# Performance work log

Measured on AMD Instinct MI355X. Metric: run time of the kernel, lower is better.

## Reference

```python
import jax, jax.numpy as jnp
import numpy as np

B, P, M, C = 64, 8732, 16, 81
THRESHOLD = 0.5
NEG_POS_RATIO = 3
ALPHA = 1.0  # config.reg_weights
EPS = 1e-7


def cxcy_to_xy(c):
    return jnp.concatenate([c[..., :2] - c[..., 2:] / 2.0,
                            c[..., :2] + c[..., 2:] / 2.0], axis=-1)


def _rand_boxes_cxcy(key, shape):
    k1, k2 = jax.random.split(key)
    cxcy = jax.random.uniform(k1, shape + (2,), minval=0.2, maxval=0.8)
    wh = jax.random.uniform(k2, shape + (2,), minval=0.05, maxval=0.35)
    return jnp.concatenate([cxcy, wh], axis=-1)


def setup_inputs() -> dict:
    key = jax.random.key(0)
    ks = jax.random.split(key, 5)
    predicted_locs = cxcy_to_xy(_rand_boxes_cxcy(ks[0], (B, P)))          # valid corner boxes
    predicted_scores = jax.random.normal(ks[1], (B, P, C), dtype=jnp.float32)
    boxes = jnp.clip(cxcy_to_xy(_rand_boxes_cxcy(ks[2], (B, M))), 0.0, 1.0)  # GT corner boxes
    labels = jax.random.randint(ks[3], (B, M), 1, C)                       # object labels (1..C-1)
    priors_cxcy = _rand_boxes_cxcy(ks[4], (P,))
    return {"predicted_locs": predicted_locs, "predicted_scores": predicted_scores,
            "boxes": boxes, "labels": labels, "priors_cxcy": priors_cxcy}


def jaccard(a, b):
    # a: [M,4], b: [P,4] corner boxes -> [M,P] IoU
    lt = jnp.maximum(a[:, None, :2], b[None, :, :2])
    rb = jnp.minimum(a[:, None, 2:], b[None, :, 2:])
    wh = jnp.clip(rb - lt, 0.0)
    inter = wh[..., 0] * wh[..., 1]
    area_a = (a[:, 2] - a[:, 0]) * (a[:, 3] - a[:, 1])
    area_b = (b[:, 2] - b[:, 0]) * (b[:, 3] - b[:, 1])
    return inter / (area_a[:, None] + area_b[None, :] - inter)


def diou_loss(b1, b2):
    # corner boxes, elementwise over leading dims -> per-box loss 1 - DIoU
    lt = jnp.maximum(b1[..., :2], b2[..., :2])
    rb = jnp.minimum(b1[..., 2:], b2[..., 2:])
    wh = jnp.clip(rb - lt, 0.0)
    inter = wh[..., 0] * wh[..., 1]
    area1 = (b1[..., 2] - b1[..., 0]) * (b1[..., 3] - b1[..., 1])
    area2 = (b2[..., 2] - b2[..., 0]) * (b2[..., 3] - b2[..., 1])
    iou = inter / (area1 + area2 - inter + EPS)
    c1 = (b1[..., :2] + b1[..., 2:]) / 2.0
    c2 = (b2[..., :2] + b2[..., 2:]) / 2.0
    inter_diag = jnp.sum((c1 - c2) ** 2, axis=-1)
    enc_lt = jnp.minimum(b1[..., :2], b2[..., :2])
    enc_rb = jnp.maximum(b1[..., 2:], b2[..., 2:])
    outer_diag = jnp.sum((enc_rb - enc_lt) ** 2, axis=-1)
    dious = jnp.clip(iou - inter_diag / (outer_diag + EPS), -1.0, 1.0)
    return 1.0 - dious


def reference(predicted_locs, predicted_scores, boxes, labels, priors_cxcy):
    priors_xy = cxcy_to_xy(priors_cxcy)

    def assign(boxes_i, labels_i):
        overlap = jaccard(boxes_i, priors_xy)              # [M, P]
        ovl_prior = overlap.max(axis=0)                    # best overlap per prior
        obj_prior = overlap.argmax(axis=0)                 # best object per prior
        ovl_obj = overlap.max(axis=1)                      # best overlap per object
        prior_obj = overlap.argmax(axis=1)                 # best prior per object
        valid = ovl_obj > 0
        j_idx = jnp.cumsum(valid.astype(jnp.int32)) - 1    # index within filtered list (faithful)
        idx = jnp.where(valid, prior_obj, P)               # P -> dropped (out of bounds)
        ovl_prior = ovl_prior.at[idx].set(1.0, mode='drop')
        obj_prior = obj_prior.at[idx].set(j_idx, mode='drop')
        lab = labels_i[obj_prior]
        label_pos = jnp.where(ovl_prior < THRESHOLD, 0, lab)
        label_neg = jnp.where(ovl_prior < THRESHOLD - 0.1, -1, lab)
        return label_pos, label_neg

    true_classes, true_neg_classes = jax.vmap(assign)(boxes, labels)  # [B,P] each
    positive = true_classes > 0                                        # [B,P]
    pos_f = positive.astype(jnp.float32)
    n_pos_total = jnp.sum(pos_f)

    # Localization loss: DIoU(pred_pos, pred_pos) with reduce='mean' (faithful to source)
    per_box = diou_loss(predicted_locs, predicted_locs)                # [B,P]
    loc_loss = jnp.sum(per_box * pos_f) / jnp.maximum(n_pos_total, 1.0)

    # Confidence loss: per-prior CE + hard-negative mining (neg_pos_ratio)
    logp = jax.nn.log_softmax(predicted_scores, axis=-1)
    conf_all = -jnp.take_along_axis(logp, true_classes[..., None], axis=-1)[..., 0]  # [B,P]
    conf_pos_sum = jnp.sum(conf_all * pos_f)
    conf_neg = jnp.where(positive, 0.0, conf_all)
    conf_neg_sorted = -jnp.sort(-conf_neg, axis=-1)                    # descending
    n_hard = NEG_POS_RATIO * jnp.sum(positive, axis=1)                 # [B]
    hard_mask = (jnp.arange(P)[None, :] < n_hard[:, None]).astype(jnp.float32)
    conf_loss = (jnp.sum(conf_neg_sorted * hard_mask) + conf_pos_sum) / n_pos_total

    return conf_loss + ALPHA * loc_loss
```

## Files before the change

### kernel.cpp

```cpp
#include <hip/hip_runtime.h>
#include <math.h>

#define B_ 64
#define P_ 8732
#define M_ 16
#define C_ 81
#define THRESH 0.5f
#define EPS_ 1e-7f

#define AB_ 64
#define ROWS_PER_CHUNK 64
#define NCHUNKS ((B_ * P_) / ROWS_PER_CHUNK)
#define CHUNK_F4 (ROWS_PER_CHUNK * C_ / 4)

__global__ __launch_bounds__(256, 4) void fused_assign_lse(
    const float* __restrict__ scores,
    const float* __restrict__ boxes,
    const int*   __restrict__ labels,
    const float* __restrict__ priors,
    float*       __restrict__ lse,
    int*         __restrict__ tcls,
    int*         __restrict__ done_ctr)
{
    __shared__ __attribute__((aligned(16))) float s_buf[ROWS_PER_CHUNK * C_];
    __shared__ float s_bx[M_][4];
    __shared__ float s_barea[M_];
    __shared__ int   s_lab[M_];
    __shared__ float s_wv4[M_][4];
    __shared__ int   s_wp4[M_][4];
    __shared__ int   s_tp[M_];
    __shared__ int   s_tn;

    const int tid  = threadIdx.x;
    const int lane = tid & 63;
    const int wv   = tid >> 6;

    if (blockIdx.x < AB_) {
        const int b = blockIdx.x;
        if (b == 0 && tid == 0) *done_ctr = 0;

        if (tid < M_*4) ((float*)s_bx)[tid] = boxes[b*M_*4 + tid];
        if (tid < M_)   s_lab[tid] = labels[b*M_ + tid];
        __syncthreads();
        if (tid < M_)
            s_barea[tid] = (s_bx[tid][2]-s_bx[tid][0])*(s_bx[tid][3]-s_bx[tid][1]);
        __syncthreads();

        const float4* pri4 = (const float4*)priors;

        float bestv[M_]; int bestp[M_];
        #pragma unroll
        for (int m = 0; m < M_; ++m) { bestv[m] = -1.0f; bestp[m] = 0x7fffffff; }

        for (int p = tid; p < P_; p += 256) {
            float4 pc = pri4[p];
            float px1 = pc.x - pc.z*0.5f, py1 = pc.y - pc.w*0.5f;
            float px2 = pc.x + pc.z*0.5f, py2 = pc.y + pc.w*0.5f;
            float parea = (px2-px1)*(py2-py1);
            #pragma unroll
            for (int m = 0; m < M_; ++m) {
                float ix1 = fmaxf(s_bx[m][0], px1);
                float iy1 = fmaxf(s_bx[m][1], py1);
                float ix2 = fminf(s_bx[m][2], px2);
                float iy2 = fminf(s_bx[m][3], py2);
                float iw = fmaxf(ix2-ix1, 0.0f);
                float ih = fmaxf(iy2-iy1, 0.0f);
                float inter = iw*ih;
                float iou = inter / (s_barea[m] + parea - inter);
                if (iou > bestv[m]) { bestv[m] = iou; bestp[m] = p; }
            }
        }

        #pragma unroll
        for (int m = 0; m < M_; ++m) {
            float v = bestv[m]; int p = bestp[m];
            #pragma unroll
            for (int o = 32; o; o >>= 1) {
                float v2 = __shfl_xor(v, o);
                int   p2 = __shfl_xor(p, o);
                if (v2 > v || (v2 == v && p2 < p)) { v = v2; p = p2; }
            }
            if (lane == 0) { s_wv4[m][wv] = v; s_wp4[m][wv] = p; }
        }
        __syncthreads();

        if (tid == 0) {
            int cnt = 0;
            for (int m = 0; m < M_; ++m) {
                float v = s_wv4[m][0]; int p = s_wp4[m][0];
                #pragma unroll
                for (int w = 1; w < 4; ++w) {
                    float v2 = s_wv4[m][w]; int p2 = s_wp4[m][w];
                    if (v2 > v || (v2 == v && p2 < p)) { v = v2; p = p2; }
                }
                if (v > 0.0f) { s_tp[cnt] = p; cnt++; }
            }
            s_tn = cnt;
        }
        __syncthreads();

        const int tn = s_tn;

        for (int p = tid; p < P_; p += 256) {
            float4 pc = pri4[p];
            float px1 = pc.x - pc.z*0.5f, py1 = pc.y - pc.w*0.5f;
            float px2 = pc.x + pc.z*0.5f, py2 = pc.y + pc.w*0.5f;
            float parea = (px2-px1)*(py2-py1);
            float bv = -1.0f; int bm = 0;
            #pragma unroll
            for (int m = 0; m < M_; ++m) {
                float ix1 = fmaxf(s_bx[m][0], px1);
                float iy1 = fmaxf(s_bx[m][1], py1);
                float ix2 = fminf(s_bx[m][2], px2);
                float iy2 = fminf(s_bx[m][3], py2);
                float iw = fmaxf(ix2-ix1, 0.0f);
                float ih = fmaxf(iy2-iy1, 0.0f);
                float inter = iw*ih;
                float iou = inter / (s_barea[m] + parea - inter);
                if (iou > bv) { bv = iou; bm = m; }
            }
            int ovr = -1;
            for (int e = 0; e < tn; ++e)
                if (s_tp[e] == p) ovr = e;
            int tc = (ovr >= 0) ? s_lab[ovr]
                                : ((bv < THRESH) ? 0 : s_lab[bm]);
            tcls[(size_t)b*P_ + p] = tc;
        }
    } else {
        const int c  = blockIdx.x - AB_;
        const int s  = lane & 3;
        const int rl = (lane >> 2) + wv * 16;

        const float4* src4 = (const float4*)scores + (size_t)c * CHUNK_F4;
        float4*       dst4 = (float4*)s_buf;

        #pragma unroll
        for (int k = 0; k < 5; ++k) {
            __builtin_amdgcn_global_load_lds(
                (const __attribute__((address_space(1))) void*)(src4 + k*256 + tid),
                (__attribute__((address_space(3))) void*)(dst4 + k*256 + wv*64),
                16, 0, 0);
        }
        if (tid < 16) dst4[1280 + tid] = src4[1280 + tid];
        __syncthreads();

        const int cnt   = (s == 0) ? 21 : 20;
        const int cbase = (s == 0) ? 0  : (1 + 20 * s);

        const float* rowp = &s_buf[rl * C_ + cbase];
        float x[21];
        float mx = -INFINITY;
        #pragma unroll
        for (int k = 0; k < 21; ++k) {
            if (k < cnt) { x[k] = rowp[k]; mx = fmaxf(mx, x[k]); }
            else x[k] = -INFINITY;
        }
        mx = fmaxf(mx, __shfl_xor(mx, 1));
        mx = fmaxf(mx, __shfl_xor(mx, 2));

        float e = 0.f;
        #pragma unroll
        for (int k = 0; k < 21; ++k) e += __expf(x[k] - mx);
        e += __shfl_xor(e, 1);
        e += __shfl_xor(e, 2);

        if (s == 0)
            lse[(size_t)c * ROWS_PER_CHUNK + rl] = mx + __logf(e);
    }
}

__global__ __launch_bounds__(1024) void topk_kernel(
    const float* __restrict__ scores,
    const float* __restrict__ locs,
    const float* __restrict__ lse,
    const int*   __restrict__ tcls,
    float*       __restrict__ hard,
    float*       __restrict__ psum,
    float*       __restrict__ lsum,
    int*         __restrict__ npos,
    int*         __restrict__ done_ctr,
    float*       __restrict__ out)
{
    const int b = blockIdx.x;
    const int tid = threadIdx.x;
    const int lane = tid & 63;
    const int wv = tid >> 6;

    __shared__ float s_v[P_];
    __shared__ int   s_hist[16][256];
    __shared__ int   s_cg[257];
    __shared__ int   s_sel;
    __shared__ int   s_ct[16];
    __shared__ float s_pa[16];
    __shared__ float s_la[16];
    __shared__ int   s_rt[16];
    __shared__ float s_rf[16];
    __shared__ int   s_last;

    const size_t base = (size_t)b * P_;

    float p_acc = 0.f, l_acc = 0.f; int cpos = 0;
    for (int i = tid; i < P_; i += 1024) {
        const int t = tcls[base + i];
        const float conf = lse[base + i] - scores[(base + i) * C_ + t];
        float v;
        if (t > 0) {
            v = 0.f;
            cpos++;
            p_acc += conf;
            float4 bx = ((const float4*)locs)[base + i];
            float w = bx.z - bx.x, h = bx.w - bx.y;
            float iw = fmaxf(w, 0.f), ih = fmaxf(h, 0.f);
            float inter = iw * ih;
            float area  = w * h;
            float iou   = inter / (area + area - inter + EPS_);
            float diou  = fminf(fmaxf(iou, -1.f), 1.f);
            l_acc += 1.f - diou;
        } else {
            v = fmaxf(conf, 0.f);
        }
        s_v[i] = v;
    }

    #pragma unroll
    for (int o = 32; o; o >>= 1) {
        cpos  += __shfl_xor(cpos, o);
        p_acc += __shfl_xor(p_acc, o);
        l_acc += __shfl_xor(l_acc, o);
    }
    if (lane == 0) { s_ct[wv] = cpos; s_pa[wv] = p_acc; s_la[wv] = l_acc; }
    __syncthreads();

    int cp_tot = 0;
    #pragma unroll
    for (int w = 0; w < 16; ++w) cp_tot += s_ct[w];
    int k = 3 * cp_tot;
    if (k > P_) k = P_;

    float hsum = 0.f;
    if (k > 0) {
        const unsigned masks[4]  = {0u, 0xFF800000u, 0xFFFF8000u, 0xFFFFFF80u};
        const int      shifts[4] = {23, 15, 7, 0};

        unsigned prefix = 0u;
        int k_rem = k;

        for (int rd = 0; rd < 4; ++rd) {
            const unsigned hm = masks[rd];
            const int sh = shifts[rd];

            ((int*)s_hist)[tid] = 0;
            ((int*)s_hist)[tid + 1024] = 0;
            ((int*)s_hist)[tid + 2048] = 0;
            ((int*)s_hist)[tid + 3072] = 0;
            __syncthreads();

            for (int i = tid; i < P_; i += 1024) {
                unsigned u = __float_as_uint(s_v[i]);
                if ((u & hm) == prefix)
                    atomicAdd(&s_hist[wv][(u >> sh) & 0xFF], 1);
            }
            __syncthreads();

            if (wv == 0) {
                int carry = 0;
                for (int cbin = 3; cbin >= 0; --cbin) {
                    int bin = cbin * 64 + lane;
                    int tot = 0;
                    #pragma unroll
                    for (int w = 0; w < 16; ++w) tot += s_hist[w][bin];
                    #pragma unroll
                    for (int o = 1; o < 64; o <<= 1) {
                        int v = __shfl_down(tot, o);
                        if (lane + o < 64) tot += v;
                    }
                    int cg = tot + carry;
                    s_cg[bin] = cg;
                    carry = __shfl(cg, 0);
                }
                if (lane == 0) s_cg[256] = 0;
            }
            __syncthreads();

            if (tid < 256) {
                if (s_cg[tid] >= k_rem && s_cg[tid + 1] < k_rem) s_sel = tid;
            }
            __syncthreads();

            const int bsel = s_sel;
            k_rem -= s_cg[bsel + 1];
            prefix |= (unsigned)bsel << sh;
            __syncthreads();
        }

        const float tval = __uint_as_float(prefix);

        float sum = 0.f; int cgt = 0;
        for (int i = tid; i < P_; i += 1024) {
            float v = s_v[i];
            if (v > tval) { sum += v; cgt++; }
        }
        #pragma unroll
        for (int o = 32; o; o >>= 1) { sum += __shfl_xor(sum, o); cgt += __shfl_xor(cgt, o); }
        if (lane == 0) { s_rf[wv] = sum; s_rt[wv] = cgt; }
        __syncthreads();
        if (tid == 0) {
            float ssum = 0.f; int cc = 0;
            #pragma unroll
            for (int w = 0; w < 16; ++w) { ssum += s_rf[w]; cc += s_rt[w]; }
            hsum = ssum + (float)(k - cc) * tval;
        }
    }

    if (tid == 0) {
        float pt = 0.f, lt = 0.f;
        #pragma unroll
        for (int w = 0; w < 16; ++w) { pt += s_pa[w]; lt += s_la[w]; }
        atomicExch(&hard[b], hsum);
        atomicExch(&psum[b], pt);
        atomicExch(&lsum[b], lt);
        atomicExch(&npos[b], cp_tot);
        __threadfence();
        s_last = (atomicAdd(done_ctr, 1) == B_ - 1) ? 1 : 0;
    }
    __syncthreads();

    if (s_last && wv == 0) {
        __threadfence();
        double h  = (double)atomicAdd(&hard[lane], 0.0f);
        double p  = (double)atomicAdd(&psum[lane], 0.0f);
        double l  = (double)atomicAdd(&lsum[lane], 0.0f);
        double np = (double)atomicAdd(&npos[lane], 0);
        #pragma unroll
        for (int o = 32; o; o >>= 1) {
            h += __shfl_xor(h, o); p += __shfl_xor(p, o);
            l += __shfl_xor(l, o); np += __shfl_xor(np, o);
        }
        if (lane == 0) {
            double conf_loss = (h + p) / np;
            double loc_loss  = l / fmax(np, 1.0);
            out[0] = (float)(conf_loss + 1.0 * loc_loss);
        }
    }
}

extern "C" void kernel_launch(void* const* d_in, const int* in_sizes, int n_in,
                              void* d_out, int out_size, void* d_ws, size_t ws_size,
                              hipStream_t stream) {
    const float* predicted_locs   = (const float*)d_in[0];
    const float* predicted_scores = (const float*)d_in[1];
    const float* boxes            = (const float*)d_in[2];
    const int*   labels           = (const int*)d_in[3];
    const float* priors           = (const float*)d_in[4];
    float* out = (float*)d_out;

    char* ws = (char*)d_ws;
    size_t off = 0;
    float* lse      = (float*)(ws + off); off += sizeof(float) * (size_t)B_ * P_;
    int*   tcls     = (int*)(ws + off);   off += sizeof(int)   * (size_t)B_ * P_;
    float* hard     = (float*)(ws + off); off += sizeof(float) * B_;
    float* psum     = (float*)(ws + off); off += sizeof(float) * B_;
    float* lsum     = (float*)(ws + off); off += sizeof(float) * B_;
    int*   npos     = (int*)(ws + off);   off += sizeof(int)   * B_;
    int*   done_ctr = (int*)(ws + off);   off += sizeof(int)   * 4;

    fused_assign_lse<<<AB_ + NCHUNKS, 256, 0, stream>>>(
        predicted_scores, boxes, labels, priors, lse, tcls, done_ctr);
    topk_kernel<<<B_, 1024, 0, stream>>>(
        predicted_scores, predicted_locs, lse, tcls,
        hard, psum, lsum, npos, done_ctr, out);
}
```

Baseline: 395.7 us.

## Use persistent blocks with atomic work-stealing and double-buffered LDS prefetch for LSE

```diff
diff --git a/kernel.cpp b/kernel.cpp
--- a/kernel.cpp
+++ b/kernel.cpp
@@ -12,17 +12,23 @@
 #define ROWS_PER_CHUNK 64
 #define NCHUNKS ((B_ * P_) / ROWS_PER_CHUNK)
 #define CHUNK_F4 (ROWS_PER_CHUNK * C_ / 4)
-
-__global__ __launch_bounds__(256, 4) void fused_assign_lse(
+#define GRID_CE 768
+#define GRAB 4
+
+__global__ void init_kernel(int* __restrict__ ctrs) {
+    if (threadIdx.x < 2) ctrs[threadIdx.x] = 0;
+}
+
+__global__ __launch_bounds__(256, 3) void fused_assign_lse(
     const float* __restrict__ scores,
     const float* __restrict__ boxes,
     const int*   __restrict__ labels,
     const float* __restrict__ priors,
     float*       __restrict__ lse,
     int*         __restrict__ tcls,
-    int*         __restrict__ done_ctr)
+    int*         __restrict__ ctrs)
 {
-    __shared__ __attribute__((aligned(16))) float s_buf[ROWS_PER_CHUNK * C_];
+    __shared__ __attribute__((aligned(16))) float s_buf[2][ROWS_PER_CHUNK * C_];
     __shared__ float s_bx[M_][4];
     __shared__ float s_barea[M_];
     __shared__ int   s_lab[M_];
@@ -30,6 +36,7 @@
     __shared__ int   s_wp4[M_][4];
     __shared__ int   s_tp[M_];
     __shared__ int   s_tn;
+    __shared__ int   s_grab;
 
     const int tid  = threadIdx.x;
     const int lane = tid & 63;
@@ -37,7 +44,6 @@
 
     if (blockIdx.x < AB_) {
         const int b = blockIdx.x;
-        if (b == 0 && tid == 0) *done_ctr = 0;
 
         if (tid < M_*4) ((float*)s_bx)[tid] = boxes[b*M_*4 + tid];
         if (tid < M_)   s_lab[tid] = labels[b*M_ + tid];
@@ -126,46 +132,85 @@
                                 : ((bv < THRESH) ? 0 : s_lab[bm]);
             tcls[(size_t)b*P_ + p] = tc;
         }
-    } else {
-        const int c  = blockIdx.x - AB_;
-        const int s  = lane & 3;
-        const int rl = (lane >> 2) + wv * 16;
-
-        const float4* src4 = (const float4*)scores + (size_t)c * CHUNK_F4;
-        float4*       dst4 = (float4*)s_buf;
-
-        #pragma unroll
-        for (int k = 0; k < 5; ++k) {
-            __builtin_amdgcn_global_load_lds(
-                (const __attribute__((address_space(1))) void*)(src4 + k*256 + tid),
-                (__attribute__((address_space(3))) void*)(dst4 + k*256 + wv*64),
-                16, 0, 0);
-        }
-        if (tid < 16) dst4[1280 + tid] = src4[1280 + tid];
-        __syncthreads();
-
-        const int cnt   = (s == 0) ? 21 : 20;
-        const int cbase = (s == 0) ? 0  : (1 + 20 * s);
-
-        const float* rowp = &s_buf[rl * C_ + cbase];
-        float x[21];
-        float mx = -INFINITY;
-        #pragma unroll
-        for (int k = 0; k < 21; ++k) {
-            if (k < cnt) { x[k] = rowp[k]; mx = fmaxf(mx, x[k]); }
-            else x[k] = -INFINITY;
-        }
-        mx = fmaxf(mx, __shfl_xor(mx, 1));
-        mx = fmaxf(mx, __shfl_xor(mx, 2));
-
-        float e = 0.f;
-        #pragma unroll
-        for (int k = 0; k < 21; ++k) e += __expf(x[k] - mx);
-        e += __shfl_xor(e, 1);
-        e += __shfl_xor(e, 2);
-
-        if (s == 0)
-            lse[(size_t)c * ROWS_PER_CHUNK + rl] = mx + __logf(e);
+        __syncthreads();
+    }
+
+    const int s  = lane & 3;
+    const int rl = (lane >> 2) + wv * 16;
+    const int cnt   = (s == 0) ? 21 : 20;
+    const int cbase = (s == 0) ? 0  : (1 + 20 * s);
+    const float4* sc4 = (const float4*)scores;
+
+    if (tid == 0) s_grab = atomicAdd(&ctrs[0], GRAB);
+    __syncthreads();
+    int g = s_grab;
+    int cur = 0;
+
+    while (g < NCHUNKS) {
+        const int gend = min(g + GRAB, NCHUNKS);
+
+        {
+            const float4* src4 = sc4 + (size_t)g * CHUNK_F4;
+            float4*       dst4 = (float4*)s_buf[cur];
+            #pragma unroll
+            for (int k = 0; k < 5; ++k) {
+                __builtin_amdgcn_global_load_lds(
+                    (const __attribute__((address_space(1))) void*)(src4 + k*256 + tid),
+                    (__attribute__((address_space(3))) void*)(dst4 + k*256 + wv*64),
+                    16, 0, 0);
+            }
+            if (tid < 16) dst4[1280 + tid] = src4[1280 + tid];
+        }
+        __syncthreads();
+
+        for (int c = g; ; ) {
+            const int  cn       = c + 1;
+            const bool boundary = (cn >= gend);
+            float4 tail;
+
+            if (!boundary) {
+                const float4* src4 = sc4 + (size_t)cn * CHUNK_F4;
+                float4*       dst4 = (float4*)s_buf[cur ^ 1];
+                #pragma unroll
+                for (int k = 0; k < 5; ++k) {
+                    __builtin_amdgcn_global_load_lds(
+                        (const __attribute__((address_space(1))) void*)(src4 + k*256 + tid),
+                        (__attribute__((address_space(3))) void*)(dst4 + k*256 + wv*64),
+                        16, 0, 0);
+                }
+                if (tid < 16) tail = src4[1280 + tid];
+            } else {
+                if (tid == 0) s_grab = atomicAdd(&ctrs[0], GRAB);
+            }
+
+            const float* rowp = &s_buf[cur][rl * C_ + cbase];
+            float x[21];
+            float mx = -INFINITY;
+            #pragma unroll
+            for (int k = 0; k < 21; ++k) {
+                if (k < cnt) { x[k] = rowp[k]; mx = fmaxf(mx, x[k]); }
+                else x[k] = -INFINITY;
+            }
+            mx = fmaxf(mx, __shfl_xor(mx, 1));
+            mx = fmaxf(mx, __shfl_xor(mx, 2));
+
+            float e = 0.f;
+            #pragma unroll
+            for (int k = 0; k < 21; ++k) e += __expf(x[k] - mx);
+            e += __shfl_xor(e, 1);
+            e += __shfl_xor(e, 2);
+
+            if (s == 0)
+                lse[(size_t)c * ROWS_PER_CHUNK + rl] = mx + __logf(e);
+
+            if (!boundary && tid < 16)
+                ((float4*)s_buf[cur ^ 1])[1280 + tid] = tail;
+
+            __syncthreads();
+            if (boundary) break;
+            c = cn; cur ^= 1;
+        }
+        g = s_grab;
     }
 }
 
@@ -178,7 +223,7 @@
     float*       __restrict__ psum,
     float*       __restrict__ lsum,
     int*         __restrict__ npos,
-    int*         __restrict__ done_ctr,
+    int*         __restrict__ ctrs,
     float*       __restrict__ out)
 {
     const int b = blockIdx.x;
@@ -321,7 +366,7 @@
         atomicExch(&lsum[b], lt);
         atomicExch(&npos[b], cp_tot);
         __threadfence();
-        s_last = (atomicAdd(done_ctr, 1) == B_ - 1) ? 1 : 0;
+        s_last = (atomicAdd(&ctrs[1], 1) == B_ - 1) ? 1 : 0;
     }
     __syncthreads();
 
@@ -362,11 +407,12 @@
     float* psum     = (float*)(ws + off); off += sizeof(float) * B_;
     float* lsum     = (float*)(ws + off); off += sizeof(float) * B_;
     int*   npos     = (int*)(ws + off);   off += sizeof(int)   * B_;
-    int*   done_ctr = (int*)(ws + off);   off += sizeof(int)   * 4;
-
-    fused_assign_lse<<<AB_ + NCHUNKS, 256, 0, stream>>>(
-        predicted_scores, boxes, labels, priors, lse, tcls, done_ctr);
+    int*   ctrs     = (int*)(ws + off);   off += sizeof(int)   * 4;
+
+    init_kernel<<<1, 64, 0, stream>>>(ctrs);
+    fused_assign_lse<<<GRID_CE, 256, 0, stream>>>(
+        predicted_scores, boxes, labels, priors, lse, tcls, ctrs);
     topk_kernel<<<B_, 1024, 0, stream>>>(
         predicted_scores, predicted_locs, lse, tcls,
-        hard, psum, lsum, npos, done_ctr, out);
+        hard, psum, lsum, npos, ctrs, out);
 }
```

After: 368.8 us. 6.8% less time.
